# Optimization experiments

Measured on AMD Instinct MI355X. Metric: run time of the kernel, lower is better.

The kernel has to match this reference:

```python
import jax, jax.numpy as jnp
import numpy as np

NEG_SLOPE = 0.2

def gat_conv(x, src, dst, n, W, att_src, att_dst, bias, heads, out_ch, concat):
    # x: [N, F_in]; W: [heads*out_ch, F_in]; att_*: [heads, out_ch]; bias: [heads*out_ch] or [out_ch]
    h = (x @ W.T).reshape(n, heads, out_ch)              # [N,H,C]
    a_src = jnp.einsum('nhc,hc->nh', h, att_src)          # [N,H]
    a_dst = jnp.einsum('nhc,hc->nh', h, att_dst)          # [N,H]
    alpha = jax.nn.leaky_relu(a_src[src] + a_dst[dst], NEG_SLOPE)  # [E,H]
    # segment softmax over incoming edges of each destination node
    amax = jax.ops.segment_max(alpha, dst, num_segments=n)         # [N,H]
    amax = jnp.where(jnp.isfinite(amax), amax, 0.0)
    ex = jnp.exp(alpha - amax[dst])                                # [E,H]
    denom = jax.ops.segment_sum(ex, dst, num_segments=n)           # [N,H]
    w = ex / (denom[dst] + 1e-16)                                  # [E,H]
    out = jax.ops.segment_sum(w[:, :, None] * h[src], dst, num_segments=n)  # [N,H,C]
    if concat:
        out = out.reshape(n, heads * out_ch)
    else:
        out = out.mean(axis=1)
    return out + bias


def setup_inputs() -> dict:
    key = jax.random.key(0)
    ks = jax.random.split(key, 16)
    n, E = 10000, 320000
    in_dim, hid, heads = 128, 128, 4
    sc = lambda f: 1.0 / np.sqrt(f)
    x = jax.random.normal(ks[0], (n, in_dim), dtype=jnp.float32)
    edge_index = jax.random.randint(ks[1], (2, E), 0, n, dtype=jnp.int64)
    # layer 0: in_dim -> hid, heads=4, concat
    W0 = jax.random.normal(ks[2], (heads * hid, in_dim), jnp.float32) * sc(in_dim)
    att_src0 = jax.random.normal(ks[3], (heads, hid), jnp.float32) * sc(hid)
    att_dst0 = jax.random.normal(ks[4], (heads, hid), jnp.float32) * sc(hid)
    b0 = jnp.zeros((heads * hid,), jnp.float32)
    # layer 1: hid*heads -> hid, heads=1, concat
    W1 = jax.random.normal(ks[5], (hid, heads * hid), jnp.float32) * sc(heads * hid)
    att_src1 = jax.random.normal(ks[6], (1, hid), jnp.float32) * sc(hid)
    att_dst1 = jax.random.normal(ks[7], (1, hid), jnp.float32) * sc(hid)
    b1 = jnp.zeros((hid,), jnp.float32)
    Wout = jax.random.normal(ks[8], (hid, hid), jnp.float32) * sc(hid)
    bout = jnp.zeros((hid,), jnp.float32)
    Wedge = jax.random.normal(ks[9], (1, 2 * hid), jnp.float32) * sc(2 * hid)
    bedge = jnp.zeros((1,), jnp.float32)
    return {"x": x, "edge_index": edge_index, "W0": W0, "att_src0": att_src0,
            "att_dst0": att_dst0, "b0": b0, "W1": W1, "att_src1": att_src1,
            "att_dst1": att_dst1, "b1": b1, "Wout": Wout, "bout": bout,
            "Wedge": Wedge, "bedge": bedge}


def reference(x, edge_index, W0, att_src0, att_dst0, b0, W1, att_src1, att_dst1,
              b1, Wout, bout, Wedge, bedge):
    n = x.shape[0]
    hid = Wout.shape[0]
    # add self-loops (PyG GATConv default)
    loop = jnp.arange(n, dtype=edge_index.dtype)
    src = jnp.concatenate([edge_index[0], loop])
    dst = jnp.concatenate([edge_index[1], loop])
    h = jax.nn.elu(gat_conv(x, src, dst, n, W0, att_src0, att_dst0, b0, 4, hid, True))
    h = jax.nn.elu(gat_conv(h, src, dst, n, W1, att_src1, att_dst1, b1, 1, hid, True))
    h = h @ Wout.T + bout                                  # [n, hid]
    # edge_proj(cat(x_i, x_j)) == x_i @ w1 + x_j @ w2 + b  (avoid [n,n,2h] materialization)
    w1 = Wedge[0, :hid]
    w2 = Wedge[0, hid:]
    s1 = h @ w1                                            # [n]
    s2 = h @ w2                                            # [n]
    edge_logits = s1[:, None] + s2[None, :] + bedge[0]     # [n, n]
    return edge_logits
```

## Files before the change

kernel.cpp:

```cpp
#include <hip/hip_runtime.h>
#include <math.h>

#define LRELU_SLOPE 0.2f

__device__ __forceinline__ float lrelu(float x){ return x >= 0.f ? x : LRELU_SLOPE*x; }
__device__ __forceinline__ float eluf(float x){ return x > 0.f ? x : expm1f(x); }

__global__ void k_hist(const int* __restrict__ ei, int E, int n, int* __restrict__ cnt){
    int e = blockIdx.x*blockDim.x + threadIdx.x;
    int NE = E + n;
    if (e >= NE) return;
    int d = (e < E) ? ei[E + e] : (e - E);
    atomicAdd(&cnt[d], 1);
}

__global__ __launch_bounds__(1024) void k_scan(const int* __restrict__ cnt, int n,
                                               int* __restrict__ off, int* __restrict__ cur){
    __shared__ int part[1024];
    const int ITEMS = (n + 1023) / 1024;
    int t = threadIdx.x;
    int base = t * ITEMS;
    int s = 0;
    for (int i = 0; i < ITEMS; i++){ int idx = base + i; if (idx < n) s += cnt[idx]; }
    part[t] = s;
    __syncthreads();
    for (int d = 1; d < 1024; d <<= 1){
        int v = 0;
        if (t >= d) v = part[t - d];
        __syncthreads();
        if (t >= d) part[t] += v;
        __syncthreads();
    }
    int excl = part[t] - s;
    for (int i = 0; i < ITEMS; i++){
        int idx = base + i;
        if (idx < n){ off[idx] = excl; cur[idx] = excl; excl += cnt[idx]; }
    }
    if (t == 1023) off[n] = part[1023];
}

__global__ void k_scatter(const int* __restrict__ ei, int E, int n,
                          int* __restrict__ cur, int* __restrict__ esrc){
    int e = blockIdx.x*blockDim.x + threadIdx.x;
    int NE = E + n;
    if (e >= NE) return;
    int s = (e < E) ? ei[e]     : (e - E);
    int d = (e < E) ? ei[E + e] : (e - E);
    int pos = atomicAdd(&cur[d], 1);
    esrc[pos] = s;
}

__global__ __launch_bounds__(256) void k_gemm_nt(
    const float* __restrict__ A, const float* __restrict__ B,
    const float* __restrict__ bias, float* __restrict__ C,
    int M, int N, int K)
{
    const int BM = 64, BN = 64, BK = 32, PAD = 4;
    __shared__ float As[BK][BM + PAD];
    __shared__ float Bs[BK][BN + PAD];
    int tid = threadIdx.x;
    int tx = tid & 15;
    int ty = tid >> 4;
    int m0 = blockIdx.x * BM;
    int n0 = blockIdx.y * BN;
    float acc[4][4] = {};

    int lm = tid >> 3;
    int lk = (tid & 7) * 4;

    for (int k0 = 0; k0 < K; k0 += BK){
        #pragma unroll
        for (int r = 0; r < 2; r++){
            int m = lm + 32*r;
            int row = m0 + m;
            float4 v = make_float4(0.f,0.f,0.f,0.f);
            if (row < M) v = *(const float4*)&A[(size_t)row*K + k0 + lk];
            As[lk+0][m] = v.x; As[lk+1][m] = v.y; As[lk+2][m] = v.z; As[lk+3][m] = v.w;
        }
        #pragma unroll
        for (int r = 0; r < 2; r++){
            int nn = lm + 32*r;
            int col = n0 + nn;
            float4 v = make_float4(0.f,0.f,0.f,0.f);
            if (col < N) v = *(const float4*)&B[(size_t)col*K + k0 + lk];
            Bs[lk+0][nn] = v.x; Bs[lk+1][nn] = v.y; Bs[lk+2][nn] = v.z; Bs[lk+3][nn] = v.w;
        }
        __syncthreads();
        #pragma unroll
        for (int kk = 0; kk < BK; kk++){
            float4 a = *(const float4*)&As[kk][tx*4];
            float4 b = *(const float4*)&Bs[kk][ty*4];
            float av[4] = {a.x,a.y,a.z,a.w};
            float bv[4] = {b.x,b.y,b.z,b.w};
            #pragma unroll
            for (int i = 0; i < 4; i++)
                #pragma unroll
                for (int j = 0; j < 4; j++)
                    acc[i][j] = fmaf(av[i], bv[j], acc[i][j]);
        }
        __syncthreads();
    }

    float4 bb = make_float4(0.f,0.f,0.f,0.f);
    if (bias) bb = *(const float4*)&bias[n0 + ty*4];
    #pragma unroll
    for (int i = 0; i < 4; i++){
        int row = m0 + tx*4 + i;
        if (row >= M) continue;
        float4 v = make_float4(acc[i][0]+bb.x, acc[i][1]+bb.y, acc[i][2]+bb.z, acc[i][3]+bb.w);
        *(float4*)&C[(size_t)row*N + n0 + ty*4] = v;
    }
}

template<int H>
__global__ __launch_bounds__(64) void k_att(
    const float* __restrict__ h, const float* __restrict__ att_s,
    const float* __restrict__ att_d, int n,
    float* __restrict__ as_, float* __restrict__ ad_)
{
    const int C = 128;
    int i = blockIdx.x;
    int l = threadIdx.x;
    const float* hrow = h + (size_t)i * H * C;
    #pragma unroll
    for (int hh = 0; hh < H; hh++){
        float h0v = hrow[hh*C + l], h1v = hrow[hh*C + l + 64];
        float ps = h0v*att_s[hh*C + l] + h1v*att_s[hh*C + l + 64];
        float pd = h0v*att_d[hh*C + l] + h1v*att_d[hh*C + l + 64];
        #pragma unroll
        for (int o = 32; o > 0; o >>= 1){ ps += __shfl_down(ps, o); pd += __shfl_down(pd, o); }
        if (l == 0){ as_[(size_t)i*H + hh] = ps; ad_[(size_t)i*H + hh] = pd; }
    }
}

template<int H, int NT>
__global__ __launch_bounds__(NT) void k_agg(
    const float* __restrict__ hfeat,
    const float* __restrict__ as_,
    const float* __restrict__ ad_,
    const int* __restrict__ off, const int* __restrict__ esrc,
    const float* __restrict__ bias,
    float* __restrict__ out, int n)
{
    const int C = 128, F = H * C;
    const int PC = F / NT;
    const int NW = NT / 64;
    int d = blockIdx.x;
    int t = threadIdx.x;
    int lane = t & 63, wv = t >> 6;
    int e0 = off[d], e1 = off[d+1];

    __shared__ float red[NW][H];
    __shared__ float m_sh[H], iden_sh[H];
    __shared__ int   src_l[64];
    __shared__ float exw[64][H];

    float adl[H];
    #pragma unroll
    for (int hh = 0; hh < H; hh++) adl[hh] = ad_[(size_t)d*H + hh];

    float mloc[H];
    #pragma unroll
    for (int hh = 0; hh < H; hh++) mloc[hh] = -1e30f;
    for (int e = e0 + t; e < e1; e += NT){
        int s = esrc[e];
        #pragma unroll
        for (int hh = 0; hh < H; hh++)
            mloc[hh] = fmaxf(mloc[hh], lrelu(as_[(size_t)s*H + hh] + adl[hh]));
    }
    #pragma unroll
    for (int hh = 0; hh < H; hh++){
        float v = mloc[hh];
        #pragma unroll
        for (int o = 32; o > 0; o >>= 1) v = fmaxf(v, __shfl_down(v, o));
        if (lane == 0) red[wv][hh] = v;
    }
    __syncthreads();
    if (t == 0){
        #pragma unroll
        for (int hh = 0; hh < H; hh++){
            float v = red[0][hh];
            for (int w = 1; w < NW; w++) v = fmaxf(v, red[w][hh]);
            m_sh[hh] = v;
        }
    }
    __syncthreads();
    float m[H];
    #pragma unroll
    for (int hh = 0; hh < H; hh++) m[hh] = m_sh[hh];

    float dloc[H];
    #pragma unroll
    for (int hh = 0; hh < H; hh++) dloc[hh] = 0.f;
    for (int e = e0 + t; e < e1; e += NT){
        int s = esrc[e];
        #pragma unroll
        for (int hh = 0; hh < H; hh++)
            dloc[hh] += expf(lrelu(as_[(size_t)s*H + hh] + adl[hh]) - m[hh]);
    }
    __syncthreads();
    #pragma unroll
    for (int hh = 0; hh < H; hh++){
        float v = dloc[hh];
        #pragma unroll
        for (int o = 32; o > 0; o >>= 1) v += __shfl_down(v, o);
        if (lane == 0) red[wv][hh] = v;
    }
    __syncthreads();
    if (t == 0){
        #pragma unroll
        for (int hh = 0; hh < H; hh++){
            float v = red[0][hh];
            for (int w = 1; w < NW; w++) v += red[w][hh];
            iden_sh[hh] = 1.f / (v + 1e-16f);
        }
    }
    __syncthreads();

    float acc[PC];
    #pragma unroll
    for (int p = 0; p < PC; p++) acc[p] = 0.f;
    for (int cb = e0; cb < e1; cb += 64){
        int ce = min(64, e1 - cb);
        if (t < 64 * H){
            int eidx = t / H, hh = t % H;
            if (eidx < ce){
                int s = esrc[cb + eidx];
                if (hh == 0) src_l[eidx] = s;
                exw[eidx][hh] = expf(lrelu(as_[(size_t)s*H + hh] + adl[hh]) - m[hh]);
            }
        }
        __syncthreads();
        for (int e = 0; e < ce; e++){
            int s = src_l[e];
            const float* hr = hfeat + (size_t)s * F;
            #pragma unroll
            for (int p = 0; p < PC; p++){
                int c = t + p * NT;
                acc[p] = fmaf(exw[e][c >> 7], hr[c], acc[p]);
            }
        }
        __syncthreads();
    }

    #pragma unroll
    for (int p = 0; p < PC; p++){
        int c = t + p * NT;
        float v = acc[p] * iden_sh[c >> 7] + bias[c];
        out[(size_t)d * F + c] = eluf(v);
    }
}

__global__ __launch_bounds__(64) void k_score(
    const float* __restrict__ h3, const float* __restrict__ wedge,
    const float* __restrict__ bedge, int n,
    float* __restrict__ s1, float* __restrict__ s2)
{
    int i = blockIdx.x, l = threadIdx.x;
    const float* hr = h3 + (size_t)i * 128;
    float h0v = hr[l], h1v = hr[l + 64];
    float p1 = h0v*wedge[l]       + h1v*wedge[l + 64];
    float p2 = h0v*wedge[128 + l] + h1v*wedge[192 + l];
    #pragma unroll
    for (int o = 32; o > 0; o >>= 1){ p1 += __shfl_down(p1, o); p2 += __shfl_down(p2, o); }
    if (l == 0){ s1[i] = p1 + bedge[0]; s2[i] = p2; }
}

__global__ __launch_bounds__(256) void k_outer(
    const float* __restrict__ s1, const float* __restrict__ s2,
    float* __restrict__ out, int n)
{
    int i = blockIdx.x;
    float a = s1[i];
    float4* orow = (float4*)(out + (size_t)i * n);
    const float4* s2v = (const float4*)s2;
    int nq = n >> 2;
    for (int j = threadIdx.x; j < nq; j += blockDim.x){
        float4 b = s2v[j];
        orow[j] = make_float4(a + b.x, a + b.y, a + b.z, a + b.w);
    }
    int rem0 = nq << 2;
    for (int j = rem0 + threadIdx.x; j < n; j += blockDim.x)
        out[(size_t)i * n + j] = a + s2[j];
}

extern "C" void kernel_launch(void* const* d_in, const int* in_sizes, int n_in,
                              void* d_out, int out_size, void* d_ws, size_t ws_size,
                              hipStream_t stream) {
    const float* x     = (const float*)d_in[0];
    const int*   ei    = (const int*)  d_in[1];
    const float* W0    = (const float*)d_in[2];
    const float* as0w  = (const float*)d_in[3];
    const float* ad0w  = (const float*)d_in[4];
    const float* b0    = (const float*)d_in[5];
    const float* W1    = (const float*)d_in[6];
    const float* as1w  = (const float*)d_in[7];
    const float* ad1w  = (const float*)d_in[8];
    const float* b1    = (const float*)d_in[9];
    const float* Wout  = (const float*)d_in[10];
    const float* boutp = (const float*)d_in[11];
    const float* Wedge = (const float*)d_in[12];
    const float* bedge = (const float*)d_in[13];

    const int hid    = in_sizes[7];
    const int heads  = in_sizes[3] / hid;
    const int in_dim = in_sizes[2] / (heads * hid);
    const int n      = in_sizes[0] / in_dim;
    const int E      = in_sizes[1] / 2;
    const int NE     = E + n;
    const int F0     = heads * hid;

    char* ws = (char*)d_ws;
    size_t pos = 0;
    auto alloc = [&](size_t bytes) -> void* {
        pos = (pos + 255) & ~size_t(255);
        void* p = ws + pos;
        pos += bytes;
        return p;
    };
    float* a0s = (float*)alloc((size_t)n * heads * 4);
    float* a0d = (float*)alloc((size_t)n * heads * 4);
    float* a1s = (float*)alloc((size_t)n * 4);
    float* a1d = (float*)alloc((size_t)n * 4);
    float* s1  = (float*)alloc((size_t)n * 4);
    float* s2  = (float*)alloc((size_t)n * 4);
    int*   cnt = (int*)  alloc((size_t)n * 4);
    int*   offs= (int*)  alloc((size_t)(n + 1) * 4);
    int*   cur = (int*)  alloc((size_t)n * 4);

    auto al = [](size_t b){ return (b + 255) & ~size_t(255); };
    size_t b_esrc = al((size_t)NE * 4);
    size_t b_h0   = al((size_t)n * F0 * 4);
    size_t b_o1   = al((size_t)n * F0 * 4);
    size_t b_h1   = al((size_t)n * hid * 4);
    size_t b_o2   = al((size_t)n * hid * 4);
    size_t b_h3   = al((size_t)n * hid * 4);
    size_t big_need = b_esrc + b_h0 + b_o1 + b_h1 + b_o2 + b_h3;
    size_t small_end = (pos + 255) & ~size_t(255);
    char* big = (small_end + big_need <= ws_size) ? (ws + small_end) : (char*)d_out;
    size_t bp = 0;
    int*   esrc = (int*)  (big + bp); bp += b_esrc;
    float* h0   = (float*)(big + bp); bp += b_h0;
    float* o1   = (float*)(big + bp); bp += b_o1;
    float* h1   = (float*)(big + bp); bp += b_h1;
    float* o2   = (float*)(big + bp); bp += b_o2;
    float* h3   = (float*)(big + bp); bp += b_h3;

    (void)hipMemsetAsync(cnt, 0, (size_t)n * 4, stream);
    int tb = 256, gbE = (NE + tb - 1) / tb;
    k_hist   <<<gbE, tb, 0, stream>>>(ei, E, n, cnt);
    k_scan   <<<1, 1024, 0, stream>>>(cnt, n, offs, cur);
    k_scatter<<<gbE, tb, 0, stream>>>(ei, E, n, cur, esrc);

    int gx = (n + 63) / 64;

    k_gemm_nt<<<dim3(gx, F0/64), 256, 0, stream>>>(x, W0, nullptr, h0, n, F0, in_dim);
    k_att<4> <<<n, 64, 0, stream>>>(h0, as0w, ad0w, n, a0s, a0d);
    k_agg<4, 256><<<n, 256, 0, stream>>>(h0, a0s, a0d, offs, esrc, b0, o1, n);

    k_gemm_nt<<<dim3(gx, hid/64), 256, 0, stream>>>(o1, W1, nullptr, h1, n, hid, F0);
    k_att<1> <<<n, 64, 0, stream>>>(h1, as1w, ad1w, n, a1s, a1d);
    k_agg<1, 128><<<n, 128, 0, stream>>>(h1, a1s, a1d, offs, esrc, b1, o2, n);

    k_gemm_nt<<<dim3(gx, hid/64), 256, 0, stream>>>(o2, Wout, boutp, h3, n, hid, hid);

    k_score<<<n, 64, 0, stream>>>(h3, Wedge, bedge, n, s1, s2);
    k_outer<<<n, 256, 0, stream>>>(s1, s2, (float*)d_out, n);
}
```

Measured before the change: 689.7 us.

## Single-pass GAT aggregation without max subtraction, split edges across waves

The aggregation kernels now compute the softmax in one pass. Exponentials are clamped at 80 instead of subtracting a per-node max, so the two extra passes over incoming edges are gone. Edges are distributed across wavefronts with vectorized float4 feature gathers, and per-wave partial sums are reduced in shared memory at the end. The attention-score and edge-score kernels use wider vector loads with xor shuffles, and the large outer-product output uses nontemporal stores. Dropping the max subtraction changes numerics and could lose precision or saturate if logits were large.

```diff
diff --git a/kernel.cpp b/kernel.cpp
--- a/kernel.cpp
+++ b/kernel.cpp
@@ -2,6 +2,8 @@
 #include <math.h>
 
 #define LRELU_SLOPE 0.2f
+
+typedef float f32x4 __attribute__((ext_vector_type(4)));
 
 __device__ __forceinline__ float lrelu(float x){ return x >= 0.f ? x : LRELU_SLOPE*x; }
 __device__ __forceinline__ float eluf(float x){ return x > 0.f ? x : expm1f(x); }
@@ -112,29 +114,45 @@
     }
 }
 
-template<int H>
-__global__ __launch_bounds__(64) void k_att(
+__global__ __launch_bounds__(64) void k_att4(
     const float* __restrict__ h, const float* __restrict__ att_s,
     const float* __restrict__ att_d, int n,
     float* __restrict__ as_, float* __restrict__ ad_)
 {
-    const int C = 128;
-    int i = blockIdx.x;
-    int l = threadIdx.x;
-    const float* hrow = h + (size_t)i * H * C;
-    #pragma unroll
-    for (int hh = 0; hh < H; hh++){
-        float h0v = hrow[hh*C + l], h1v = hrow[hh*C + l + 64];
-        float ps = h0v*att_s[hh*C + l] + h1v*att_s[hh*C + l + 64];
-        float pd = h0v*att_d[hh*C + l] + h1v*att_d[hh*C + l + 64];
-        #pragma unroll
-        for (int o = 32; o > 0; o >>= 1){ ps += __shfl_down(ps, o); pd += __shfl_down(pd, o); }
-        if (l == 0){ as_[(size_t)i*H + hh] = ps; ad_[(size_t)i*H + hh] = pd; }
-    }
-}
-
-template<int H, int NT>
-__global__ __launch_bounds__(NT) void k_agg(
+    int i = blockIdx.x, l = threadIdx.x;
+    const float4* hr = (const float4*)(h + (size_t)i * 512);
+    float4 v0 = hr[l*2], v1 = hr[l*2 + 1];
+    int hh = l >> 4;
+    const float4* sp = (const float4*)(att_s + hh*128 + (l & 15)*8);
+    const float4* dp = (const float4*)(att_d + hh*128 + (l & 15)*8);
+    float4 s0 = sp[0], s1v = sp[1];
+    float4 d0 = dp[0], d1v = dp[1];
+    float ps = v0.x*s0.x + v0.y*s0.y + v0.z*s0.z + v0.w*s0.w
+             + v1.x*s1v.x + v1.y*s1v.y + v1.z*s1v.z + v1.w*s1v.w;
+    float pd = v0.x*d0.x + v0.y*d0.y + v0.z*d0.z + v0.w*d0.w
+             + v1.x*d1v.x + v1.y*d1v.y + v1.z*d1v.z + v1.w*d1v.w;
+    #pragma unroll
+    for (int o = 8; o > 0; o >>= 1){ ps += __shfl_xor(ps, o); pd += __shfl_xor(pd, o); }
+    if ((l & 15) == 0){ as_[(size_t)i*4 + hh] = ps; ad_[(size_t)i*4 + hh] = pd; }
+}
+
+__global__ __launch_bounds__(64) void k_att1(
+    const float* __restrict__ h, const float* __restrict__ att_s,
+    const float* __restrict__ att_d, int n,
+    float* __restrict__ as_, float* __restrict__ ad_)
+{
+    int i = blockIdx.x, l = threadIdx.x;
+    float2 v  = ((const float2*)(h + (size_t)i * 128))[l];
+    float2 s  = ((const float2*)att_s)[l];
+    float2 dd = ((const float2*)att_d)[l];
+    float ps = v.x*s.x + v.y*s.y;
+    float pd = v.x*dd.x + v.y*dd.y;
+    #pragma unroll
+    for (int o = 32; o > 0; o >>= 1){ ps += __shfl_xor(ps, o); pd += __shfl_xor(pd, o); }
+    if (l == 0){ as_[i] = ps; ad_[i] = pd; }
+}
+
+__global__ __launch_bounds__(256) void k_agg4(
     const float* __restrict__ hfeat,
     const float* __restrict__ as_,
     const float* __restrict__ ad_,
@@ -142,112 +160,138 @@
     const float* __restrict__ bias,
     float* __restrict__ out, int n)
 {
-    const int C = 128, F = H * C;
-    const int PC = F / NT;
-    const int NW = NT / 64;
-    int d = blockIdx.x;
-    int t = threadIdx.x;
+    const int CH = 128;
+    int d = blockIdx.x, t = threadIdx.x;
     int lane = t & 63, wv = t >> 6;
+
+    __shared__ int   src_l[CH];
+    __shared__ float exw[CH][4];
+    __shared__ float dsum[4];
+    __shared__ __align__(16) float part[4][512];
+
     int e0 = off[d], e1 = off[d+1];
 
-    __shared__ float red[NW][H];
-    __shared__ float m_sh[H], iden_sh[H];
-    __shared__ int   src_l[64];
-    __shared__ float exw[64][H];
-
-    float adl[H];
-    #pragma unroll
-    for (int hh = 0; hh < H; hh++) adl[hh] = ad_[(size_t)d*H + hh];
-
-    float mloc[H];
-    #pragma unroll
-    for (int hh = 0; hh < H; hh++) mloc[hh] = -1e30f;
-    for (int e = e0 + t; e < e1; e += NT){
-        int s = esrc[e];
+    float ad0 = ad_[(size_t)d*4+0], ad1 = ad_[(size_t)d*4+1],
+          ad2 = ad_[(size_t)d*4+2], ad3 = ad_[(size_t)d*4+3];
+
+    float acc[8];
+    #pragma unroll
+    for (int j = 0; j < 8; j++) acc[j] = 0.f;
+    float dtot = 0.f;
+
+    for (int cb = e0; cb < e1; cb += CH){
+        int ce = min(CH, e1 - cb);
+        for (int e = t; e < ce; e += 256){
+            int s = esrc[cb + e];
+            src_l[e] = s;
+            float4 a4 = ((const float4*)as_)[s];
+            exw[e][0] = expf(fminf(lrelu(a4.x + ad0), 80.f));
+            exw[e][1] = expf(fminf(lrelu(a4.y + ad1), 80.f));
+            exw[e][2] = expf(fminf(lrelu(a4.z + ad2), 80.f));
+            exw[e][3] = expf(fminf(lrelu(a4.w + ad3), 80.f));
+        }
+        __syncthreads();
+        {
+            float v = 0.f;
+            for (int e = lane; e < ce; e += 64) v += exw[e][wv];
+            #pragma unroll
+            for (int o = 32; o > 0; o >>= 1) v += __shfl_xor(v, o);
+            dtot += v;
+        }
+        for (int e = wv; e < ce; e += 4){
+            int s = src_l[e];
+            float w = exw[e][lane >> 4];
+            const float4* hp = (const float4*)(hfeat + (size_t)s*512 + lane*8);
+            float4 u0 = hp[0], u1 = hp[1];
+            acc[0] = fmaf(w, u0.x, acc[0]);
+            acc[1] = fmaf(w, u0.y, acc[1]);
+            acc[2] = fmaf(w, u0.z, acc[2]);
+            acc[3] = fmaf(w, u0.w, acc[3]);
+            acc[4] = fmaf(w, u1.x, acc[4]);
+            acc[5] = fmaf(w, u1.y, acc[5]);
+            acc[6] = fmaf(w, u1.z, acc[6]);
+            acc[7] = fmaf(w, u1.w, acc[7]);
+        }
+        __syncthreads();
+    }
+
+    if (lane == 0) dsum[wv] = dtot;
+    float4* pr = (float4*)&part[wv][lane*8];
+    pr[0] = make_float4(acc[0], acc[1], acc[2], acc[3]);
+    pr[1] = make_float4(acc[4], acc[5], acc[6], acc[7]);
+    __syncthreads();
+
+    #pragma unroll
+    for (int r = 0; r < 2; r++){
+        int c = t + r*256;
+        float sgm = part[0][c] + part[1][c] + part[2][c] + part[3][c];
+        float val = sgm / (dsum[c >> 7] + 1e-16f) + bias[c];
+        out[(size_t)d*512 + c] = eluf(val);
+    }
+}
+
+__global__ __launch_bounds__(256) void k_agg1(
+    const float* __restrict__ hfeat,
+    const float* __restrict__ as_,
+    const float* __restrict__ ad_,
+    const int* __restrict__ off, const int* __restrict__ esrc,
+    const float* __restrict__ bias,
+    float* __restrict__ out, int n)
+{
+    const int CH = 128;
+    int d = blockIdx.x, t = threadIdx.x;
+    int lane = t & 63, wv = t >> 6;
+    int half = lane >> 5, l5 = lane & 31;
+
+    __shared__ int   src_l[CH];
+    __shared__ float exw1[CH];
+    __shared__ float dsum1;
+    __shared__ __align__(16) float part[8][128];
+
+    int e0 = off[d], e1 = off[d+1];
+    float adl = ad_[d];
+
+    float4 acc = make_float4(0.f, 0.f, 0.f, 0.f);
+    float dtot = 0.f;
+
+    for (int cb = e0; cb < e1; cb += CH){
+        int ce = min(CH, e1 - cb);
+        for (int e = t; e < ce; e += 256){
+            int s = esrc[cb + e];
+            src_l[e] = s;
+            exw1[e] = expf(fminf(lrelu(as_[s] + adl), 80.f));
+        }
+        __syncthreads();
+        if (wv == 0){
+            float v = 0.f;
+            for (int e = lane; e < ce; e += 64) v += exw1[e];
+            #pragma unroll
+            for (int o = 32; o > 0; o >>= 1) v += __shfl_xor(v, o);
+            dtot += v;
+        }
+        int p = wv*2 + half;
+        for (int e = p; e < ce; e += 8){
+            int s = src_l[e];
+            float w = exw1[e];
+            float4 u = *(const float4*)(hfeat + (size_t)s*128 + l5*4);
+            acc.x = fmaf(w, u.x, acc.x);
+            acc.y = fmaf(w, u.y, acc.y);
+            acc.z = fmaf(w, u.z, acc.z);
+            acc.w = fmaf(w, u.w, acc.w);
+        }
+        __syncthreads();
+    }
+
+    if (t == 0) dsum1 = dtot;
+    ((float4*)&part[wv*2 + half][0])[l5] = acc;
+    __syncthreads();
+
+    if (t < 128){
+        float sgm = 0.f;
         #pragma unroll
-        for (int hh = 0; hh < H; hh++)
-            mloc[hh] = fmaxf(mloc[hh], lrelu(as_[(size_t)s*H + hh] + adl[hh]));
-    }
-    #pragma unroll
-    for (int hh = 0; hh < H; hh++){
-        float v = mloc[hh];
-        #pragma unroll
-        for (int o = 32; o > 0; o >>= 1) v = fmaxf(v, __shfl_down(v, o));
-        if (lane == 0) red[wv][hh] = v;
-    }
-    __syncthreads();
-    if (t == 0){
-        #pragma unroll
-        for (int hh = 0; hh < H; hh++){
-            float v = red[0][hh];
-            for (int w = 1; w < NW; w++) v = fmaxf(v, red[w][hh]);
-            m_sh[hh] = v;
-        }
-    }
-    __syncthreads();
-    float m[H];
-    #pragma unroll
-    for (int hh = 0; hh < H; hh++) m[hh] = m_sh[hh];
-
-    float dloc[H];
-    #pragma unroll
-    for (int hh = 0; hh < H; hh++) dloc[hh] = 0.f;
-    for (int e = e0 + t; e < e1; e += NT){
-        int s = esrc[e];
-        #pragma unroll
-        for (int hh = 0; hh < H; hh++)
-            dloc[hh] += expf(lrelu(as_[(size_t)s*H + hh] + adl[hh]) - m[hh]);
-    }
-    __syncthreads();
-    #pragma unroll
-    for (int hh = 0; hh < H; hh++){
-        float v = dloc[hh];
-        #pragma unroll
-        for (int o = 32; o > 0; o >>= 1) v += __shfl_down(v, o);
-        if (lane == 0) red[wv][hh] = v;
-    }
-    __syncthreads();
-    if (t == 0){
-        #pragma unroll
-        for (int hh = 0; hh < H; hh++){
-            float v = red[0][hh];
-            for (int w = 1; w < NW; w++) v += red[w][hh];
-            iden_sh[hh] = 1.f / (v + 1e-16f);
-        }
-    }
-    __syncthreads();
-
-    float acc[PC];
-    #pragma unroll
-    for (int p = 0; p < PC; p++) acc[p] = 0.f;
-    for (int cb = e0; cb < e1; cb += 64){
-        int ce = min(64, e1 - cb);
-        if (t < 64 * H){
-            int eidx = t / H, hh = t % H;
-            if (eidx < ce){
-                int s = esrc[cb + eidx];
-                if (hh == 0) src_l[eidx] = s;
-                exw[eidx][hh] = expf(lrelu(as_[(size_t)s*H + hh] + adl[hh]) - m[hh]);
-            }
-        }
-        __syncthreads();
-        for (int e = 0; e < ce; e++){
-            int s = src_l[e];
-            const float* hr = hfeat + (size_t)s * F;
-            #pragma unroll
-            for (int p = 0; p < PC; p++){
-                int c = t + p * NT;
-                acc[p] = fmaf(exw[e][c >> 7], hr[c], acc[p]);
-            }
-        }
-        __syncthreads();
-    }
-
-    #pragma unroll
-    for (int p = 0; p < PC; p++){
-        int c = t + p * NT;
-        float v = acc[p] * iden_sh[c >> 7] + bias[c];
-        out[(size_t)d * F + c] = eluf(v);
+        for (int p = 0; p < 8; p++) sgm += part[p][t];
+        float val = sgm / (dsum1 + 1e-16f) + bias[t];
+        out[(size_t)d*128 + t] = eluf(val);
     }
 }
 
@@ -257,12 +301,13 @@
     float* __restrict__ s1, float* __restrict__ s2)
 {
     int i = blockIdx.x, l = threadIdx.x;
-    const float* hr = h3 + (size_t)i * 128;
-    float h0v = hr[l], h1v = hr[l + 64];
-    float p1 = h0v*wedge[l]       + h1v*wedge[l + 64];
-    float p2 = h0v*wedge[128 + l] + h1v*wedge[192 + l];
-    #pragma unroll
-    for (int o = 32; o > 0; o >>= 1){ p1 += __shfl_down(p1, o); p2 += __shfl_down(p2, o); }
+    float2 v  = ((const float2*)(h3 + (size_t)i * 128))[l];
+    float2 w1 = ((const float2*)wedge)[l];
+    float2 w2 = ((const float2*)(wedge + 128))[l];
+    float p1 = v.x*w1.x + v.y*w1.y;
+    float p2 = v.x*w2.x + v.y*w2.y;
+    #pragma unroll
+    for (int o = 32; o > 0; o >>= 1){ p1 += __shfl_xor(p1, o); p2 += __shfl_xor(p2, o); }
     if (l == 0){ s1[i] = p1 + bedge[0]; s2[i] = p2; }
 }
 
@@ -272,12 +317,13 @@
 {
     int i = blockIdx.x;
     float a = s1[i];
-    float4* orow = (float4*)(out + (size_t)i * n);
-    const float4* s2v = (const float4*)s2;
+    f32x4* orow = (f32x4*)(out + (size_t)i * n);
+    const f32x4* s2v = (const f32x4*)s2;
     int nq = n >> 2;
     for (int j = threadIdx.x; j < nq; j += blockDim.x){
-        float4 b = s2v[j];
-        orow[j] = make_float4(a + b.x, a + b.y, a + b.z, a + b.w);
+        f32x4 b = s2v[j];
+        f32x4 r = b + a;
+        __builtin_nontemporal_store(r, &orow[j]);
     }
     int rem0 = nq << 2;
     for (int j = rem0 + threadIdx.x; j < n; j += blockDim.x)
@@ -355,12 +401,12 @@
     int gx = (n + 63) / 64;
 
     k_gemm_nt<<<dim3(gx, F0/64), 256, 0, stream>>>(x, W0, nullptr, h0, n, F0, in_dim);
-    k_att<4> <<<n, 64, 0, stream>>>(h0, as0w, ad0w, n, a0s, a0d);
-    k_agg<4, 256><<<n, 256, 0, stream>>>(h0, a0s, a0d, offs, esrc, b0, o1, n);
+    k_att4   <<<n, 64, 0, stream>>>(h0, as0w, ad0w, n, a0s, a0d);
+    k_agg4   <<<n, 256, 0, stream>>>(h0, a0s, a0d, offs, esrc, b0, o1, n);
 
     k_gemm_nt<<<dim3(gx, hid/64), 256, 0, stream>>>(o1, W1, nullptr, h1, n, hid, F0);
-    k_att<1> <<<n, 64, 0, stream>>>(h1, as1w, ad1w, n, a1s, a1d);
-    k_agg<1, 128><<<n, 128, 0, stream>>>(h1, a1s, a1d, offs, esrc, b1, o2, n);
+    k_att1   <<<n, 64, 0, stream>>>(h1, as1w, ad1w, n, a1s, a1d);
+    k_agg1   <<<n, 256, 0, stream>>>(h1, a1s, a1d, offs, esrc, b1, o2, n);
 
     k_gemm_nt<<<dim3(gx, hid/64), 256, 0, stream>>>(o2, Wout, boutp, h3, n, hid, hid);
 
```

After: 684.6 us. About the same (-0.7%).
